# Kernel tuning notes

Measured on AMD Instinct MI355X. Metric: run time of the kernel, lower is better.

## Reference

```python
import jax, jax.numpy as jnp
import numpy as np

D_MODEL = 1024
N_HEAD = 16
HEAD_D = D_MODEL // N_HEAD
D_FF = 4096
LN_EPS = 1e-5
ATTN_EPS = 1e-6


def _layer_norm(x, g, b, eps=LN_EPS):
    mu = jnp.mean(x, axis=-1, keepdims=True)
    var = jnp.var(x, axis=-1, keepdims=True)
    return (x - mu) * jax.lax.rsqrt(var + eps) * g + b


def setup_inputs() -> dict:
    key = jax.random.key(0)
    ks = jax.random.split(key, 16)
    s = 0.02
    return {
        "src": jax.random.normal(ks[0], (4, 4096, D_MODEL), dtype=jnp.float32),
        "qkv_w": jax.random.normal(ks[1], (D_MODEL, 3 * D_MODEL), dtype=jnp.float32) * s,
        "qkv_b": jax.random.normal(ks[2], (3 * D_MODEL,), dtype=jnp.float32) * s,
        "out_w": jax.random.normal(ks[3], (D_MODEL, D_MODEL), dtype=jnp.float32) * s,
        "out_b": jax.random.normal(ks[4], (D_MODEL,), dtype=jnp.float32) * s,
        "w1": jax.random.normal(ks[5], (D_MODEL, D_FF), dtype=jnp.float32) * s,
        "b1": jax.random.normal(ks[6], (D_FF,), dtype=jnp.float32) * s,
        "w2": jax.random.normal(ks[7], (D_FF, D_MODEL), dtype=jnp.float32) * s,
        "b2": jax.random.normal(ks[8], (D_MODEL,), dtype=jnp.float32) * s,
        "g1": jnp.ones((D_MODEL,), dtype=jnp.float32),
        "be1": jnp.zeros((D_MODEL,), dtype=jnp.float32),
        "g2": jnp.ones((D_MODEL,), dtype=jnp.float32),
        "be2": jnp.zeros((D_MODEL,), dtype=jnp.float32),
    }


def _linear_attention(x, qkv_w, qkv_b, out_w, out_b):
    B, N, C = x.shape
    qkv = (x @ qkv_w + qkv_b).reshape(B, N, 3, N_HEAD, HEAD_D)
    qkv = jnp.transpose(qkv, (2, 0, 3, 1, 4))  # [3,B,H,N,D]
    q, k, v = qkv[0], qkv[1], qkv[2]
    # phi = elu(x) + 1 (positive feature map)
    qf = jax.nn.elu(q) + 1.0
    kf = jax.nn.elu(k) + 1.0
    # kv aggregation: [B,H,D,D]
    kv = jnp.einsum('bhnd,bhne->bhde', kf.astype(jnp.float32), v.astype(jnp.float32)).astype(v.dtype)
    y_num = jnp.einsum('bhnd,bhde->bhne', qf, kv)  # [B,H,N,D]
    z = jnp.sum(kf.astype(jnp.float32), axis=2)  # [B,H,D]
    y_den = jnp.einsum('bhnd,bhd->bhn', qf, z.astype(qf.dtype))
    y_den = jnp.maximum(y_den, ATTN_EPS)[..., None]
    y = (y_num / y_den).transpose(0, 2, 1, 3).reshape(B, N, C)
    return y @ out_w + out_b


def reference(src, qkv_w, qkv_b, out_w, out_b, w1, b1, w2, b2, g1, be1, g2, be2):
    # pre-norm (norm_first=True), dropout disabled (eval)
    attn_out = _linear_attention(_layer_norm(src, g1, be1), qkv_w, qkv_b, out_w, out_b)
    x = src + attn_out
    h = jax.nn.gelu(_layer_norm(x, g2, be2) @ w1 + b1, approximate=False)
    return x + h @ w2 + b2
```

## Files before the change

### kernel.cpp

```cpp
#include <hip/hip_runtime.h>
#include <hip/hip_bf16.h>
#include <math.h>

typedef __attribute__((ext_vector_type(8))) short short8;
typedef __attribute__((ext_vector_type(4))) float floatx4;

__device__ __forceinline__ float bf2f(unsigned int u) {
    union { unsigned int i; float f; } c; c.i = u << 16; return c.f;
}
__device__ __forceinline__ unsigned short f2bf(float f) {
    unsigned int x = __builtin_bit_cast(unsigned int, f);
    unsigned int r = (x + 0x7fffu + ((x >> 16) & 1u)) >> 16;
    return (unsigned short)r;
}
__device__ __forceinline__ float elu1(float x) { return x > 0.f ? x + 1.f : __expf(x); }
__device__ __forceinline__ float gelu_fast(float x) {
    float u = x * (1.f + 0.044715f * x * x);
    return x / (1.f + __expf(-1.5957691216f * u));
}

__device__ __forceinline__ void async_cp16(const void* g, void* l) {
    __builtin_amdgcn_global_load_lds(
        (const __attribute__((address_space(1))) unsigned int*)g,
        (__attribute__((address_space(3))) unsigned int*)l, 16, 0, 0);
}

__global__ void prep_kernel(const float* __restrict__ qkv_w, const float* __restrict__ out_w,
                            const float* __restrict__ w1, const float* __restrict__ w2,
                            unsigned short* __restrict__ qkvwT, unsigned short* __restrict__ outwT,
                            unsigned short* __restrict__ w1T, unsigned short* __restrict__ w2T,
                            float* __restrict__ kvz) {
    const int bid = blockIdx.x;
    const int tx = threadIdx.x, ty = threadIdx.y;
    if (bid >= 12288) {
        const int lid = ty * 32 + tx;
        const int i = (bid - 12288) * 1024 + lid * 4;
        *(float4*)(kvz + i) = make_float4(0.f, 0.f, 0.f, 0.f);
        return;
    }
    const float* in;
    unsigned short* op;
    int K, N, tb;
    if (bid < 3072)      { in = qkv_w; op = qkvwT; K = 1024; N = 3072; tb = bid; }
    else if (bid < 4096) { in = out_w; op = outwT; K = 1024; N = 1024; tb = bid - 3072; }
    else if (bid < 8192) { in = w1;    op = w1T;   K = 1024; N = 4096; tb = bid - 4096; }
    else                 { in = w2;    op = w2T;   K = 4096; N = 1024; tb = bid - 8192; }
    const int nx = N >> 5;
    const int n0 = (tb % nx) * 32, k0 = (tb / nx) * 32;
    __shared__ float tile[32][33];
#pragma unroll
    for (int i = 0; i < 4; i++)
        tile[ty + 8 * i][tx] = in[(size_t)(k0 + ty + 8 * i) * N + n0 + tx];
    __syncthreads();
#pragma unroll
    for (int i = 0; i < 4; i++)
        op[(size_t)(n0 + ty + 8 * i) * K + k0 + tx] = f2bf(tile[tx][ty + 8 * i]);
}

template <int IN_BF16>
__global__ __launch_bounds__(256)
void ln_kernel(const void* __restrict__ xv, const float* __restrict__ g,
               const float* __restrict__ be, unsigned short* __restrict__ out) {
    const int row = blockIdx.x;
    const int t = threadIdx.x;
    float4 v;
    if (IN_BF16) {
        const unsigned short* x = (const unsigned short*)xv;
        uint2 r = *(const uint2*)(x + (size_t)row * 1024 + t * 4);
        v.x = bf2f(r.x & 0xffff); v.y = bf2f(r.x >> 16);
        v.z = bf2f(r.y & 0xffff); v.w = bf2f(r.y >> 16);
    } else {
        v = *(const float4*)((const float*)xv + (size_t)row * 1024 + t * 4);
    }
    float s = v.x + v.y + v.z + v.w;
    float s2 = v.x * v.x + v.y * v.y + v.z * v.z + v.w * v.w;
#pragma unroll
    for (int off = 32; off > 0; off >>= 1) {
        s += __shfl_down(s, off);
        s2 += __shfl_down(s2, off);
    }
    __shared__ float red[8];
    __shared__ float stat[2];
    const int w = t >> 6, l = t & 63;
    if (l == 0) { red[w] = s; red[4 + w] = s2; }
    __syncthreads();
    if (t == 0) {
        float S = red[0] + red[1] + red[2] + red[3];
        float S2 = red[4] + red[5] + red[6] + red[7];
        float mu = S * (1.f / 1024.f);
        float var = S2 * (1.f / 1024.f) - mu * mu;
        stat[0] = mu;
        stat[1] = rsqrtf(var + 1e-5f);
    }
    __syncthreads();
    const float mu = stat[0], rs = stat[1];
    const float4 gv = *(const float4*)(g + t * 4);
    const float4 bv = *(const float4*)(be + t * 4);
    unsigned int o0 = f2bf((v.x - mu) * rs * gv.x + bv.x);
    unsigned int o1 = f2bf((v.y - mu) * rs * gv.y + bv.y);
    unsigned int o2 = f2bf((v.z - mu) * rs * gv.z + bv.z);
    unsigned int o3 = f2bf((v.w - mu) * rs * gv.w + bv.w);
    uint2 pk;
    pk.x = o0 | (o1 << 16);
    pk.y = o2 | (o3 << 16);
    *(uint2*)(out + (size_t)row * 1024 + t * 4) = pk;
}

template <int EPI>
__global__ __launch_bounds__(256, 4)
void gemm_bt(const unsigned short* __restrict__ A, const unsigned short* __restrict__ B,
             const float* __restrict__ bias, const float* __restrict__ resid,
             const unsigned short* __restrict__ residb,
             unsigned short* __restrict__ Cbf, float* __restrict__ Cf32,
             int N, int K) {
    __shared__ unsigned short At[128 * 64];
    __shared__ unsigned short Bt[128 * 64];
    const int t = threadIdx.x;
    const int l = t & 63;
    const int w = t >> 6;

    const int f = blockIdx.y * gridDim.x + blockIdx.x;
    int bx = blockIdx.x, by = blockIdx.y;
    if (gridDim.y == 128 && (gridDim.x & 3) == 0) {
        const int xcd = f & 7;
        const int g = f >> 3;
        const int nin = g & 3;
        const int r = (g >> 2) & 15;
        const int nchunk = g >> 6;
        bx = nchunk * 4 + nin;
        by = xcd * 16 + r;
    }
    const int m0 = by * 128;
    const int n0 = bx * 128;
    const int wm = (w >> 1) * 64;
    const int wn = (w & 1) * 64;

    floatx4 acc[4][4];
    const floatx4 zz = {0.f, 0.f, 0.f, 0.f};
#pragma unroll
    for (int i = 0; i < 4; i++)
#pragma unroll
        for (int j = 0; j < 4; j++) acc[i][j] = zz;

    const int sr = t >> 3;
    const int sg = ((t & 7) ^ ((t >> 3) & 7));
    const unsigned short* ag = A + (size_t)(m0 + sr) * K + sg * 8;
    const unsigned short* bg = B + (size_t)(n0 + sr) * K + sg * 8;
    unsigned short* la = At + t * 8;
    unsigned short* lb = Bt + t * 8;

    const int fr = l & 15;
    const int fx = fr & 7;
    const int g0 = (l >> 4);

    for (int k0 = 0; k0 < K; k0 += 64) {
#pragma unroll
        for (int c = 0; c < 4; c++) {
            async_cp16(ag + k0 + (size_t)(c * 32) * K, la + c * 2048);
            async_cp16(bg + k0 + (size_t)(c * 32) * K, lb + c * 2048);
        }
        __syncthreads();
#pragma unroll
        for (int sub = 0; sub < 2; sub++) {
            const int fo = ((sub * 4 + g0) ^ fx) << 3;
            short8 af[4], bf[4];
#pragma unroll
            for (int i = 0; i < 4; i++)
                af[i] = *(const short8*)(At + (wm + i * 16 + fr) * 64 + fo);
#pragma unroll
            for (int i = 0; i < 4; i++)
                bf[i] = *(const short8*)(Bt + (wn + i * 16 + fr) * 64 + fo);
#pragma unroll
            for (int i = 0; i < 4; i++)
#pragma unroll
                for (int j = 0; j < 4; j++)
                    acc[i][j] = __builtin_amdgcn_mfma_f32_16x16x32_bf16(af[i], bf[j], acc[i][j], 0, 0, 0);
        }
        __syncthreads();
    }

    const int er = (l >> 4) << 2;
    const int ec = l & 15;
#pragma unroll
    for (int j = 0; j < 4; j++) {
        const int col = n0 + wn + j * 16 + ec;
        const float bb = bias[col];
#pragma unroll
        for (int i = 0; i < 4; i++) {
            const int rowb = m0 + wm + i * 16 + er;
#pragma unroll
            for (int r = 0; r < 4; r++) {
                const int row = rowb + r;
                float v = acc[i][j][r] + bb;
                const size_t idx = (size_t)row * N + col;
                if (EPI == 0) {
                    if (col < 2048) v = elu1(v);
                    Cbf[idx] = f2bf(v);
                } else if (EPI == 2) {
                    Cbf[idx] = f2bf(gelu_fast(v));
                } else if (EPI == 3) {
                    Cbf[idx] = f2bf(v + resid[idx]);
                } else {
                    Cf32[idx] = v + bf2f(residb[idx]);
                }
            }
        }
    }
}

__global__ __launch_bounds__(256)
void kv_kernel(const unsigned short* __restrict__ qkv, float* __restrict__ kvz) {
    const int bh = blockIdx.x;
    const int chunk = blockIdx.y;
    const int b = bh >> 4, h = bh & 15;
    const int t = threadIdx.x;
    __shared__ float kf[64][68];
    __shared__ float vv[64][68];
    const int te = t >> 4, td = t & 15;
    float acc[4][4];
#pragma unroll
    for (int i = 0; i < 4; i++)
#pragma unroll
        for (int j = 0; j < 4; j++) acc[i][j] = 0.f;
    float zacc = 0.f;
    const size_t base = (size_t)b * 4096 * 3072 + (size_t)chunk * 512 * 3072;
    const int koff = 1024 + h * 64;
    const int voff = 2048 + h * 64;
    const int rl = t >> 3, seg = t & 7;

    for (int s = 0; s < 8; s++) {
#pragma unroll
        for (int p = 0; p < 2; p++) {
            const int nl = p * 32 + rl;
            const unsigned short* rp = qkv + base + (size_t)(s * 64 + nl) * 3072;
            const uint4 kd = *(const uint4*)(rp + koff + seg * 8);
            const uint4 vd = *(const uint4*)(rp + voff + seg * 8);
            float* kdst = &kf[nl][seg * 8];
            float* vdst = &vv[nl][seg * 8];
            kdst[0] = bf2f(kd.x & 0xffff); kdst[1] = bf2f(kd.x >> 16);
            kdst[2] = bf2f(kd.y & 0xffff); kdst[3] = bf2f(kd.y >> 16);
            kdst[4] = bf2f(kd.z & 0xffff); kdst[5] = bf2f(kd.z >> 16);
            kdst[6] = bf2f(kd.w & 0xffff); kdst[7] = bf2f(kd.w >> 16);
            vdst[0] = bf2f(vd.x & 0xffff); vdst[1] = bf2f(vd.x >> 16);
            vdst[2] = bf2f(vd.y & 0xffff); vdst[3] = bf2f(vd.y >> 16);
            vdst[4] = bf2f(vd.z & 0xffff); vdst[5] = bf2f(vd.z >> 16);
            vdst[6] = bf2f(vd.w & 0xffff); vdst[7] = bf2f(vd.w >> 16);
        }
        __syncthreads();
        for (int n = 0; n < 64; n++) {
            const float4 kk = *(const float4*)&kf[n][te * 4];
            const float4 vn = *(const float4*)&vv[n][td * 4];
            const float ka[4] = {kk.x, kk.y, kk.z, kk.w};
            const float va[4] = {vn.x, vn.y, vn.z, vn.w};
#pragma unroll
            for (int i = 0; i < 4; i++)
#pragma unroll
                for (int j = 0; j < 4; j++) acc[i][j] = fmaf(ka[i], va[j], acc[i][j]);
        }
        if (t < 64) {
            for (int n = 0; n < 64; n++) zacc += kf[n][t];
        }
        __syncthreads();
    }
    float* kvp = kvz + bh * 4160;
#pragma unroll
    for (int i = 0; i < 4; i++)
#pragma unroll
        for (int j = 0; j < 4; j++)
            atomicAdd(&kvp[(te * 4 + i) * 64 + td * 4 + j], acc[i][j]);
    if (t < 64) atomicAdd(&kvp[4096 + t], zacc);
}

__global__ __launch_bounds__(256)
void y_kernel(const unsigned short* __restrict__ qkv, const float* __restrict__ kvz,
              unsigned short* __restrict__ y) {
    const int bh = blockIdx.x, chunk = blockIdx.y;
    const int b = bh >> 4, h = bh & 15;
    const int t = threadIdx.x;
    __shared__ float kv[64][68];
    __shared__ float zs[64];
    __shared__ float qf[16][68];
    const float* kvp = kvz + bh * 4160;
#pragma unroll
    for (int p = 0; p < 4; p++) {
        const int f = (t + p * 256) * 4;
        const float4 v4 = *(const float4*)(kvp + f);
        *(float4*)&kv[f >> 6][f & 63] = v4;
    }
    if (t < 16) *(float4*)&zs[t * 4] = *(const float4*)(kvp + 4096 + t * 4);
    __syncthreads();
    const int nl = t >> 4, td = t & 15;
    const size_t base = (size_t)b * 4096 * 3072 + (size_t)chunk * 128 * 3072;
    const int qoff = h * 64;
    for (int s = 0; s < 8; s++) {
        if (t < 128) {
            const int r = t >> 3, seg = t & 7;
            const uint4 qd = *(const uint4*)(qkv + base + (size_t)(s * 16 + r) * 3072 + qoff + seg * 8);
            float* qdst = &qf[r][seg * 8];
            qdst[0] = bf2f(qd.x & 0xffff); qdst[1] = bf2f(qd.x >> 16);
            qdst[2] = bf2f(qd.y & 0xffff); qdst[3] = bf2f(qd.y >> 16);
            qdst[4] = bf2f(qd.z & 0xffff); qdst[5] = bf2f(qd.z >> 16);
            qdst[6] = bf2f(qd.w & 0xffff); qdst[7] = bf2f(qd.w >> 16);
        }
        __syncthreads();
        float a0 = 0.f, a1 = 0.f, a2 = 0.f, a3 = 0.f, den = 0.f;
        for (int e = 0; e < 64; e++) {
            const float q = qf[nl][e];
            const float4 kvv = *(const float4*)&kv[e][td * 4];
            a0 = fmaf(q, kvv.x, a0);
            a1 = fmaf(q, kvv.y, a1);
            a2 = fmaf(q, kvv.z, a2);
            a3 = fmaf(q, kvv.w, a3);
            den = fmaf(q, zs[e], den);
        }
        const float inv = 1.f / fmaxf(den, 1e-6f);
        const int tok = b * 4096 + chunk * 128 + s * 16 + nl;
        unsigned int o0 = f2bf(a0 * inv), o1 = f2bf(a1 * inv);
        unsigned int o2 = f2bf(a2 * inv), o3 = f2bf(a3 * inv);
        uint2 pk;
        pk.x = o0 | (o1 << 16);
        pk.y = o2 | (o3 << 16);
        *(uint2*)(y + (size_t)tok * 1024 + h * 64 + td * 4) = pk;
        __syncthreads();
    }
}

extern "C" void kernel_launch(void* const* d_in, const int* in_sizes, int n_in,
                              void* d_out, int out_size, void* d_ws, size_t ws_size,
                              hipStream_t stream) {
    const float* src   = (const float*)d_in[0];
    const float* qkv_w = (const float*)d_in[1];
    const float* qkv_b = (const float*)d_in[2];
    const float* out_w = (const float*)d_in[3];
    const float* out_b = (const float*)d_in[4];
    const float* w1    = (const float*)d_in[5];
    const float* b1    = (const float*)d_in[6];
    const float* w2    = (const float*)d_in[7];
    const float* b2    = (const float*)d_in[8];
    const float* g1    = (const float*)d_in[9];
    const float* be1   = (const float*)d_in[10];
    const float* g2    = (const float*)d_in[11];
    const float* be2   = (const float*)d_in[12];
    float* outp = (float*)d_out;

    char* ws = (char*)d_ws;
    unsigned short* qkvwT = (unsigned short*)(ws + 0);
    unsigned short* outwT = (unsigned short*)(ws + 6291456);
    unsigned short* w1T   = (unsigned short*)(ws + 8388608);
    unsigned short* w2T   = (unsigned short*)(ws + 16777216);
    unsigned short* bufA  = (unsigned short*)(ws + 25165824);
    unsigned short* bufB  = (unsigned short*)(ws + 159383552);
    unsigned short* xbuf  = (unsigned short*)(ws + 192937984);
    float*          kvz   = (float*)(ws + 260046848);

    prep_kernel<<<12548, dim3(32, 8), 0, stream>>>(qkv_w, out_w, w1, w2,
                                                   qkvwT, outwT, w1T, w2T, kvz);

    ln_kernel<0><<<16384, 256, 0, stream>>>(src, g1, be1, bufB);
    gemm_bt<0><<<dim3(24, 128), 256, 0, stream>>>(bufB, qkvwT, qkv_b, nullptr, nullptr, bufA, nullptr, 3072, 1024);
    kv_kernel<<<dim3(64, 8), 256, 0, stream>>>(bufA, kvz);
    y_kernel<<<dim3(64, 32), 256, 0, stream>>>(bufA, kvz, bufB);
    gemm_bt<3><<<dim3(8, 128), 256, 0, stream>>>(bufB, outwT, out_b, src, nullptr, xbuf, nullptr, 1024, 1024);
    ln_kernel<1><<<16384, 256, 0, stream>>>(xbuf, g2, be2, bufB);
    gemm_bt<2><<<dim3(32, 128), 256, 0, stream>>>(bufB, w1T, b1, nullptr, nullptr, bufA, nullptr, 4096, 1024);
    gemm_bt<4><<<dim3(8, 128), 256, 0, stream>>>(bufA, w2T, b2, nullptr, xbuf, nullptr, outp, 1024, 4096);
}
```

Before: 779.9 us.

## Stage GEMM epilogues through LDS for coalesced stores; fold LN1 into prep kernel

The GEMM epilogue now writes accumulator tiles into shared memory (padded stride 132) and then stores them to global memory as 16-byte vectors, replacing scattered 2- and 4-byte per-element stores. The fp32 residual epilogue does this in two halves so the tile fits in LDS. The first LayerNorm is merged into the weight-prep launch as extra blocks, removing one kernel launch. In exchange the epilogue needs more LDS and extra barriers, and in the out-projection path bias is now rounded to bf16 before the residual add, adding a second rounding step.

```diff
diff --git a/kernel.cpp b/kernel.cpp
--- a/kernel.cpp
+++ b/kernel.cpp
@@ -29,11 +29,49 @@
                             const float* __restrict__ w1, const float* __restrict__ w2,
                             unsigned short* __restrict__ qkvwT, unsigned short* __restrict__ outwT,
                             unsigned short* __restrict__ w1T, unsigned short* __restrict__ w2T,
-                            float* __restrict__ kvz) {
+                            float* __restrict__ kvz,
+                            const float* __restrict__ src, const float* __restrict__ g1,
+                            const float* __restrict__ be1, unsigned short* __restrict__ ln1out) {
     const int bid = blockIdx.x;
     const int tx = threadIdx.x, ty = threadIdx.y;
+    const int lid = ty * 32 + tx;
+    if (bid >= 12548) {
+        const int row = bid - 12548;
+        const int t = lid;
+        const float4 v = *(const float4*)(src + (size_t)row * 1024 + t * 4);
+        float s = v.x + v.y + v.z + v.w;
+        float s2 = v.x * v.x + v.y * v.y + v.z * v.z + v.w * v.w;
+#pragma unroll
+        for (int off = 32; off > 0; off >>= 1) {
+            s += __shfl_down(s, off);
+            s2 += __shfl_down(s2, off);
+        }
+        __shared__ float red[8];
+        __shared__ float stat[2];
+        const int w = t >> 6, l = t & 63;
+        if (l == 0) { red[w] = s; red[4 + w] = s2; }
+        __syncthreads();
+        if (t == 0) {
+            float S = red[0] + red[1] + red[2] + red[3];
+            float S2 = red[4] + red[5] + red[6] + red[7];
+            float mu = S * (1.f / 1024.f);
+            float var = S2 * (1.f / 1024.f) - mu * mu;
+            stat[0] = mu;
+            stat[1] = rsqrtf(var + 1e-5f);
+        }
+        __syncthreads();
+        const float mu = stat[0], rs = stat[1];
+        const float4 gv = *(const float4*)(g1 + t * 4);
+        const float4 bv = *(const float4*)(be1 + t * 4);
+        uint2 pk;
+        pk.x = (unsigned int)f2bf((v.x - mu) * rs * gv.x + bv.x) |
+               ((unsigned int)f2bf((v.y - mu) * rs * gv.y + bv.y) << 16);
+        pk.y = (unsigned int)f2bf((v.z - mu) * rs * gv.z + bv.z) |
+               ((unsigned int)f2bf((v.w - mu) * rs * gv.w + bv.w) << 16);
+        *(uint2*)(ln1out + (size_t)row * 1024 + t * 4) = pk;
+        return;
+    }
     if (bid >= 12288) {
-        const int lid = ty * 32 + tx;
         const int i = (bid - 12288) * 1024 + lid * 4;
         *(float4*)(kvz + i) = make_float4(0.f, 0.f, 0.f, 0.f);
         return;
@@ -57,20 +95,16 @@
         op[(size_t)(n0 + ty + 8 * i) * K + k0 + tx] = f2bf(tile[tx][ty + 8 * i]);
 }
 
-template <int IN_BF16>
 __global__ __launch_bounds__(256)
-void ln_kernel(const void* __restrict__ xv, const float* __restrict__ g,
+void ln_kernel(const unsigned short* __restrict__ x, const float* __restrict__ g,
                const float* __restrict__ be, unsigned short* __restrict__ out) {
     const int row = blockIdx.x;
     const int t = threadIdx.x;
     float4 v;
-    if (IN_BF16) {
-        const unsigned short* x = (const unsigned short*)xv;
+    {
         uint2 r = *(const uint2*)(x + (size_t)row * 1024 + t * 4);
         v.x = bf2f(r.x & 0xffff); v.y = bf2f(r.x >> 16);
         v.z = bf2f(r.y & 0xffff); v.w = bf2f(r.y >> 16);
-    } else {
-        v = *(const float4*)((const float*)xv + (size_t)row * 1024 + t * 4);
     }
     float s = v.x + v.y + v.z + v.w;
     float s2 = v.x * v.x + v.y * v.y + v.z * v.z + v.w * v.w;
@@ -96,13 +130,11 @@
     const float mu = stat[0], rs = stat[1];
     const float4 gv = *(const float4*)(g + t * 4);
     const float4 bv = *(const float4*)(be + t * 4);
-    unsigned int o0 = f2bf((v.x - mu) * rs * gv.x + bv.x);
-    unsigned int o1 = f2bf((v.y - mu) * rs * gv.y + bv.y);
-    unsigned int o2 = f2bf((v.z - mu) * rs * gv.z + bv.z);
-    unsigned int o3 = f2bf((v.w - mu) * rs * gv.w + bv.w);
     uint2 pk;
-    pk.x = o0 | (o1 << 16);
-    pk.y = o2 | (o3 << 16);
+    pk.x = (unsigned int)f2bf((v.x - mu) * rs * gv.x + bv.x) |
+           ((unsigned int)f2bf((v.y - mu) * rs * gv.y + bv.y) << 16);
+    pk.y = (unsigned int)f2bf((v.z - mu) * rs * gv.z + bv.z) |
+           ((unsigned int)f2bf((v.w - mu) * rs * gv.w + bv.w) << 16);
     *(uint2*)(out + (size_t)row * 1024 + t * 4) = pk;
 }
 
@@ -113,8 +145,9 @@
              const unsigned short* __restrict__ residb,
              unsigned short* __restrict__ Cbf, float* __restrict__ Cf32,
              int N, int K) {
-    __shared__ unsigned short At[128 * 64];
-    __shared__ unsigned short Bt[128 * 64];
+    __shared__ __align__(16) unsigned char smem[33792];
+    unsigned short* At = (unsigned short*)smem;
+    unsigned short* Bt = (unsigned short*)(smem + 16384);
     const int t = threadIdx.x;
     const int l = t & 63;
     const int w = t >> 6;
@@ -181,29 +214,83 @@
 
     const int er = (l >> 4) << 2;
     const int ec = l & 15;
-#pragma unroll
-    for (int j = 0; j < 4; j++) {
-        const int col = n0 + wn + j * 16 + ec;
-        const float bb = bias[col];
-#pragma unroll
-        for (int i = 0; i < 4; i++) {
-            const int rowb = m0 + wm + i * 16 + er;
-#pragma unroll
-            for (int r = 0; r < 4; r++) {
-                const int row = rowb + r;
-                float v = acc[i][j][r] + bb;
-                const size_t idx = (size_t)row * N + col;
-                if (EPI == 0) {
-                    if (col < 2048) v = elu1(v);
-                    Cbf[idx] = f2bf(v);
-                } else if (EPI == 2) {
-                    Cbf[idx] = f2bf(gelu_fast(v));
-                } else if (EPI == 3) {
-                    Cbf[idx] = f2bf(v + resid[idx]);
-                } else {
-                    Cf32[idx] = v + bf2f(residb[idx]);
+
+    if (EPI != 4) {
+        unsigned short* Ct = (unsigned short*)smem;
+#pragma unroll
+        for (int j = 0; j < 4; j++) {
+            const int lcol = wn + j * 16 + ec;
+            const float bb = bias[n0 + lcol];
+#pragma unroll
+            for (int i = 0; i < 4; i++) {
+                const int lrowb = wm + i * 16 + er;
+#pragma unroll
+                for (int r = 0; r < 4; r++) {
+                    float v = acc[i][j][r] + bb;
+                    if (EPI == 0) { if (n0 + lcol < 2048) v = elu1(v); }
+                    if (EPI == 2) v = gelu_fast(v);
+                    Ct[(lrowb + r) * 132 + lcol] = f2bf(v);
                 }
             }
+        }
+        __syncthreads();
+        const int srow = t >> 4;
+        const int scol = (t & 15) * 8;
+#pragma unroll
+        for (int it = 0; it < 8; it++) {
+            const int lrow = it * 16 + srow;
+            uint4 d = *(const uint4*)(Ct + lrow * 132 + scol);
+            if (EPI == 3) {
+                const float* rp = resid + (size_t)(m0 + lrow) * N + n0 + scol;
+                float4 r0 = *(const float4*)rp;
+                float4 r1 = *(const float4*)(rp + 4);
+                uint4 o;
+                o.x = (unsigned int)f2bf(bf2f(d.x & 0xffff) + r0.x) |
+                      ((unsigned int)f2bf(bf2f(d.x >> 16) + r0.y) << 16);
+                o.y = (unsigned int)f2bf(bf2f(d.y & 0xffff) + r0.z) |
+                      ((unsigned int)f2bf(bf2f(d.y >> 16) + r0.w) << 16);
+                o.z = (unsigned int)f2bf(bf2f(d.z & 0xffff) + r1.x) |
+                      ((unsigned int)f2bf(bf2f(d.z >> 16) + r1.y) << 16);
+                o.w = (unsigned int)f2bf(bf2f(d.w & 0xffff) + r1.z) |
+                      ((unsigned int)f2bf(bf2f(d.w >> 16) + r1.w) << 16);
+                d = o;
+            }
+            *(uint4*)(Cbf + (size_t)(m0 + lrow) * N + n0 + scol) = d;
+        }
+    } else {
+        float* Cf = (float*)smem;
+#pragma unroll
+        for (int half = 0; half < 2; half++) {
+            if ((w >> 1) == half) {
+#pragma unroll
+                for (int j = 0; j < 4; j++) {
+                    const int lcol = wn + j * 16 + ec;
+                    const float bb = bias[n0 + lcol];
+#pragma unroll
+                    for (int i = 0; i < 4; i++) {
+                        const int lrow = i * 16 + er;
+#pragma unroll
+                        for (int r = 0; r < 4; r++)
+                            Cf[(lrow + r) * 132 + lcol] = acc[i][j][r] + bb;
+                    }
+                }
+            }
+            __syncthreads();
+            const int srow = t >> 5;
+            const int scol = (t & 31) * 4;
+#pragma unroll
+            for (int it = 0; it < 8; it++) {
+                const int lrow = it * 8 + srow;
+                const int grow = m0 + half * 64 + lrow;
+                float4 v4 = *(const float4*)(Cf + lrow * 132 + scol);
+                uint2 rb = *(const uint2*)(residb + (size_t)grow * N + n0 + scol);
+                v4.x += bf2f(rb.x & 0xffff);
+                v4.y += bf2f(rb.x >> 16);
+                v4.z += bf2f(rb.y & 0xffff);
+                v4.w += bf2f(rb.y >> 16);
+                *(float4*)(Cf32 + (size_t)grow * N + n0 + scol) = v4;
+            }
+            __syncthreads();
         }
     }
 }
@@ -315,11 +402,9 @@
         }
         const float inv = 1.f / fmaxf(den, 1e-6f);
         const int tok = b * 4096 + chunk * 128 + s * 16 + nl;
-        unsigned int o0 = f2bf(a0 * inv), o1 = f2bf(a1 * inv);
-        unsigned int o2 = f2bf(a2 * inv), o3 = f2bf(a3 * inv);
         uint2 pk;
-        pk.x = o0 | (o1 << 16);
-        pk.y = o2 | (o3 << 16);
+        pk.x = (unsigned int)f2bf(a0 * inv) | ((unsigned int)f2bf(a1 * inv) << 16);
+        pk.y = (unsigned int)f2bf(a2 * inv) | ((unsigned int)f2bf(a3 * inv) << 16);
         *(uint2*)(y + (size_t)tok * 1024 + h * 64 + td * 4) = pk;
         __syncthreads();
     }
@@ -353,15 +438,15 @@
     unsigned short* xbuf  = (unsigned short*)(ws + 192937984);
     float*          kvz   = (float*)(ws + 260046848);
 
-    prep_kernel<<<12548, dim3(32, 8), 0, stream>>>(qkv_w, out_w, w1, w2,
-                                                   qkvwT, outwT, w1T, w2T, kvz);
-
-    ln_kernel<0><<<16384, 256, 0, stream>>>(src, g1, be1, bufB);
+    prep_kernel<<<28932, dim3(32, 8), 0, stream>>>(qkv_w, out_w, w1, w2,
+                                                   qkvwT, outwT, w1T, w2T, kvz,
+                                                   src, g1, be1, bufB);
+
     gemm_bt<0><<<dim3(24, 128), 256, 0, stream>>>(bufB, qkvwT, qkv_b, nullptr, nullptr, bufA, nullptr, 3072, 1024);
     kv_kernel<<<dim3(64, 8), 256, 0, stream>>>(bufA, kvz);
     y_kernel<<<dim3(64, 32), 256, 0, stream>>>(bufA, kvz, bufB);
     gemm_bt<3><<<dim3(8, 128), 256, 0, stream>>>(bufB, outwT, out_b, src, nullptr, xbuf, nullptr, 1024, 1024);
-    ln_kernel<1><<<16384, 256, 0, stream>>>(xbuf, g2, be2, bufB);
+    ln_kernel<<<16384, 256, 0, stream>>>(xbuf, g2, be2, bufB);
     gemm_bt<2><<<dim3(32, 128), 256, 0, stream>>>(bufB, w1T, b1, nullptr, nullptr, bufA, nullptr, 4096, 1024);
     gemm_bt<4><<<dim3(8, 128), 256, 0, stream>>>(bufA, w2T, b2, nullptr, xbuf, nullptr, outp, 1024, 4096);
 }
```

Result: no change. 789.4 us (+1.2%).
